# Optimization experiments

Hardware: AMD Instinct MI355X
Metric: run time of the kernel (lower is better)

## Reference

```python
import jax, jax.numpy as jnp
import numpy as np

HIDDEN = 64

def gcn_conv(x, W, b, src, dst, num_nodes):
    # GCNConv: out = D^{-1/2} (A + I) D^{-1/2} (x @ W) + b
    h = x @ W                                            # [N, F_out]
    ones = jnp.ones(src.shape[0], dtype=x.dtype)
    deg = jax.ops.segment_sum(ones, dst, num_segments=num_nodes) + 1.0  # +1 for self-loop
    dinv = jax.lax.rsqrt(deg)                             # deg^{-1/2}, deg >= 1 so safe
    norm = dinv[src] * dinv[dst]                          # [E]
    msgs = h[src] * norm[:, None]                         # [E, F_out]
    agg = jax.ops.segment_sum(msgs, dst, num_segments=num_nodes)
    # self-loop contribution: norm for (i,i) edge = dinv[i]^2
    out = agg + h * (dinv * dinv)[:, None] + b
    return out


def setup_inputs() -> dict:
    key = jax.random.key(0)
    k1, k2, k3, k4, k5 = jax.random.split(key, 5)
    N, F_in, F_out, E = 50000, 256, 128, 1600000
    x = jax.random.normal(k1, (N, F_in), dtype=jnp.float32)
    edge_index = jax.random.randint(k2, (2, E), 0, N, dtype=jnp.int64)
    W1 = jax.random.normal(k3, (F_in, HIDDEN), dtype=jnp.float32) * (1.0 / np.sqrt(F_in))
    b1 = jnp.zeros((HIDDEN,), dtype=jnp.float32)
    W2 = jax.random.normal(k4, (HIDDEN, F_out), dtype=jnp.float32) * (1.0 / np.sqrt(HIDDEN))
    b2 = jnp.zeros((F_out,), dtype=jnp.float32)
    return {"x": x, "edge_index": edge_index, "W1": W1, "b1": b1, "W2": W2, "b2": b2}


def reference(x, edge_index, W1, b1, W2, b2):
    num_nodes = x.shape[0]
    src, dst = edge_index[0], edge_index[1]
    h = gcn_conv(x, W1, b1, src, dst, num_nodes)
    h = jax.nn.relu(h)
    # dropout is identity in eval mode (training=False)
    out = gcn_conv(h, W2, b2, src, dst, num_nodes)
    return out
```

## Files before the change

kernel.cpp:

```cpp
#include <hip/hip_runtime.h>

#define FI 256
#define FH 64
#define FO 128
#define ASORT_CHUNK 2048

typedef __attribute__((ext_vector_type(8))) short bf16x8;
typedef __attribute__((ext_vector_type(4))) float f32x4;

__device__ __forceinline__ ushort f2bf(float x) {
    unsigned b = __float_as_uint(x);
    b += 0x7fffu + ((b >> 16) & 1u);
    return (ushort)(b >> 16);
}
__device__ __forceinline__ float bf2f(ushort u) {
    return __uint_as_float(((unsigned)u) << 16);
}


__global__ void zero_i32(int* __restrict__ p, int n) {
    int i = blockIdx.x * 256 + threadIdx.x;
    if (i < n) p[i] = 0;
}

__global__ void deg_cnt_kernel(const int* __restrict__ dst, int* __restrict__ cnt, int E) {
    int base = blockIdx.x * 1024 + threadIdx.x;
    #pragma unroll
    for (int q = 0; q < 4; ++q) {
        int e = base + q * 256;
        if (e < E) atomicAdd(&cnt[dst[e]], 1);
    }
}

__global__ void dinv_kernel(const int* __restrict__ cnt, float* __restrict__ dinv, int N) {
    int i = blockIdx.x * 256 + threadIdx.x;
    if (i < N) dinv[i] = rsqrtf((float)cnt[i] + 1.0f);
}


__global__ __launch_bounds__(256) void hist_wprep_kernel(const int* __restrict__ dst,
                                                         int* __restrict__ bucket_cnt,
                                                         const float* __restrict__ W1,
                                                         short* __restrict__ WH,
                                                         short* __restrict__ WL,
                                                         int E, int nblkA) {
    if ((int)blockIdx.x >= nblkA) {
        int f = ((int)blockIdx.x - nblkA) * 256 + threadIdx.x;
        float4 wv = *(const float4*)&W1[(size_t)f * 4];
        int k  = f >> 4;
        int c4 = f & 15;
        int j  = k & 7;
        int e0 = ((c4 >> 2) * 8 + (k >> 5)) * 64 + ((k >> 3) & 3) * 16 + (c4 & 3) * 4;
        float vv[4] = {wv.x, wv.y, wv.z, wv.w};
        #pragma unroll
        for (int cc = 0; cc < 4; ++cc) {
            ushort h = f2bf(vv[cc]);
            WH[(e0 + cc) * 8 + j] = (short)h;
            WL[(e0 + cc) * 8 + j] = (short)f2bf(vv[cc] - bf2f(h));
        }
        return;
    }
    __shared__ int lcnt[256];
    int t = threadIdx.x;
    int base = blockIdx.x * ASORT_CHUNK;
    lcnt[t] = 0;
    __syncthreads();
    #pragma unroll
    for (int j = 0; j < 8; ++j) {
        int e = base + j * 256 + t;
        if (e < E) atomicAdd(&lcnt[((unsigned)dst[e]) >> 8], 1);
    }
    __syncthreads();
    int v = lcnt[t];
    if (v > 0) atomicAdd(&bucket_cnt[t], v);
}

__global__ __launch_bounds__(256) void bucket_scan_kernel(const int* __restrict__ bucket_cnt,
                                                          int* __restrict__ bucket_base,
                                                          int* __restrict__ bucket_pos, int E) {
    __shared__ int sc[256];
    int t = threadIdx.x;
    int sum = bucket_cnt[t];
    sc[t] = sum;
    __syncthreads();
    for (int off = 1; off < 256; off <<= 1) {
        int u = (t >= off) ? sc[t - off] : 0;
        __syncthreads();
        sc[t] += u;
        __syncthreads();
    }
    int excl = sc[t] - sum;
    bucket_base[t] = excl;
    bucket_pos[t]  = excl;
    if (t == 255) bucket_base[256] = sc[255];
}

__global__ __launch_bounds__(256) void binA_kernel(const int* __restrict__ src,
                                                   const int* __restrict__ dst,
                                                   int* __restrict__ bucket_pos,
                                                   unsigned* __restrict__ binned, int E) {
    __shared__ int lcnt[256];
    __shared__ int lbase[256];
    __shared__ int gbase[256];
    __shared__ int sc[256];
    __shared__ unsigned sorted[ASORT_CHUNK];
    int t = threadIdx.x;
    int base = blockIdx.x * ASORT_CHUNK;
    lcnt[t] = 0;
    __syncthreads();
    unsigned pk[8];
    short bb[8];
    short mi[8];
    #pragma unroll
    for (int j = 0; j < 8; ++j) {
        int e = base + j * 256 + t;
        if (e < E) {
            unsigned s = (unsigned)src[e];
            unsigned d = (unsigned)dst[e];
            pk[j] = s | (d << 16);
            int b = (int)(d >> 8);
            bb[j] = (short)b;
            mi[j] = (short)atomicAdd(&lcnt[b], 1);
        } else {
            bb[j] = -1;
        }
    }
    __syncthreads();
    int v = lcnt[t];
    sc[t] = v;
    __syncthreads();
    #pragma unroll
    for (int off = 1; off < 256; off <<= 1) {
        int u = (t >= off) ? sc[t - off] : 0;
        __syncthreads();
        sc[t] += u;
        __syncthreads();
    }
    lbase[t] = sc[t] - v;
    if (v > 0) gbase[t] = atomicAdd(&bucket_pos[t], v);
    __syncthreads();
    #pragma unroll
    for (int j = 0; j < 8; ++j)
        if (bb[j] >= 0) sorted[lbase[(int)bb[j]] + (int)mi[j]] = pk[j];
    int tot = sc[255];
    __syncthreads();
    for (int i = t; i < tot; i += 256) {
        unsigned vv = sorted[i];
        int b = (int)(vv >> 24);
        binned[gbase[b] + (i - lbase[b])] = vv;
    }
}

__global__ __launch_bounds__(256) void binB_kernel(const int* __restrict__ bucket_base,
                                                   const unsigned* __restrict__ binned,
                                                   int* __restrict__ rec4,
                                                   int* __restrict__ row_start,
                                                   int* __restrict__ cnt,
                                                   float* __restrict__ dinv, int N) {
    __shared__ int lcnt[256];
    __shared__ int sc[256];
    __shared__ int lstart[256];
    __shared__ int loff[256];
    int t = threadIdx.x;
    int d0 = blockIdx.x << 8;
    int start = bucket_base[blockIdx.x];
    int end   = bucket_base[blockIdx.x + 1];
    lcnt[t] = 0;
    __syncthreads();
    for (int i = start + t; i < end; i += 256)
        atomicAdd(&lcnt[(binned[i] >> 16) & 0xffu], 1);
    __syncthreads();
    int v = lcnt[t];
    sc[t] = v;
    __syncthreads();
    for (int off = 1; off < 256; off <<= 1) {
        int u = (t >= off) ? sc[t - off] : 0;
        __syncthreads();
        sc[t] += u;
        __syncthreads();
    }
    int st = start + sc[t] - v;
    lstart[t] = st;
    loff[t] = 0;
    if (d0 + t < N) {
        row_start[d0 + t] = st;
        cnt[d0 + t] = v;
        dinv[d0 + t] = rsqrtf((float)v + 1.0f);
    }
    __syncthreads();
    int i = start + t;
    for (; i + 768 < end; i += 1024) {
        unsigned v0 = binned[i];
        unsigned v1 = binned[i + 256];
        unsigned v2 = binned[i + 512];
        unsigned v3 = binned[i + 768];
        int dA = (int)((v0 >> 16) & 0xffu); int kA = atomicAdd(&loff[dA], 1);
        rec4[lstart[dA] + kA] = (int)(v0 & 0xffffu);
        int dB = (int)((v1 >> 16) & 0xffu); int kB = atomicAdd(&loff[dB], 1);
        rec4[lstart[dB] + kB] = (int)(v1 & 0xffffu);
        int dC = (int)((v2 >> 16) & 0xffu); int kC = atomicAdd(&loff[dC], 1);
        rec4[lstart[dC] + kC] = (int)(v2 & 0xffffu);
        int dD = (int)((v3 >> 16) & 0xffu); int kD = atomicAdd(&loff[dD], 1);
        rec4[lstart[dD] + kD] = (int)(v3 & 0xffffu);
    }
    for (; i < end; i += 256) {
        unsigned v4 = binned[i];
        int d = (int)((v4 >> 16) & 0xffu);
        int k = atomicAdd(&loff[d], 1);
        rec4[lstart[d] + k] = (int)(v4 & 0xffffu);
    }
}


#define ACC8(hv, wt)                                                   \
    acc[0] = fmaf(__uint_as_float((hv).x << 16),         wt, acc[0]);  \
    acc[1] = fmaf(__uint_as_float((hv).x & 0xffff0000u), wt, acc[1]);  \
    acc[2] = fmaf(__uint_as_float((hv).y << 16),         wt, acc[2]);  \
    acc[3] = fmaf(__uint_as_float((hv).y & 0xffff0000u), wt, acc[3]);  \
    acc[4] = fmaf(__uint_as_float((hv).z << 16),         wt, acc[4]);  \
    acc[5] = fmaf(__uint_as_float((hv).z & 0xffff0000u), wt, acc[5]);  \
    acc[6] = fmaf(__uint_as_float((hv).w << 16),         wt, acc[6]);  \
    acc[7] = fmaf(__uint_as_float((hv).w & 0xffff0000u), wt, acc[7]);

#define GATHER_CHUNK(OFFS)                                                     \
    for (int c0 = 0; c0 < n; c0 += 64) {                                       \
        int idx_l = c0 + L;                                                    \
        int sreg = node;                                                       \
        float wreg = 0.f;                                                      \
        if (idx_l < n) {                                                       \
            sreg = rec4[beg + idx_l];                                          \
            wreg = dinv[sreg] * dvd;                                           \
        }                                                                      \
        int m = n - c0; if (m > 64) m = 64;                                    \
        int umax = (m + 7) >> 3;                                               \
        uint4 hv[8];                                                           \
        _Pragma("unroll")                                                      \
        for (int u = 0; u < 8; ++u) {                                          \
            if (u < umax) {                                                    \
                int sidx = __shfl(sreg, u * 8 + g, 64);                        \
                hv[u] = *(const uint4*)(hb + (size_t)sidx * 256 + (OFFS) + q * 8); \
            }                                                                  \
        }                                                                      \
        _Pragma("unroll")                                                      \
        for (int u = 0; u < 8; ++u) {                                          \
            if (u < umax) {                                                    \
                float wt = __shfl(wreg, u * 8 + g, 64);                        \
                ACC8(hv[u], wt)                                                \
            }                                                                  \
        }                                                                      \
    }

__global__ void gather_relu_kernel(const int* __restrict__ rec4, const int* __restrict__ row_start,
                                   const int* __restrict__ cnt, const float* __restrict__ dinv,
                                   const float* __restrict__ b1, float* __restrict__ out, int N) {
    int node = blockIdx.x * 4 + (threadIdx.x >> 6);
    if (node >= N) return;
    int L = threadIdx.x & 63;
    int g = L >> 3;
    int q = L & 7;
    const ushort* hb = (const ushort*)out;
    int beg = row_start[node];
    int n   = cnt[node];
    float dvd = dinv[node];
    float acc[8] = {0.f, 0.f, 0.f, 0.f, 0.f, 0.f, 0.f, 0.f};
    GATHER_CHUNK(128)
    #pragma unroll
    for (int off = 8; off < 64; off <<= 1)
        #pragma unroll
        for (int j = 0; j < 8; ++j)
            acc[j] += __shfl_xor(acc[j], off, 64);
    if (L < 8) {
        float dv2 = dvd * dvd;
        uint4 ho = *(const uint4*)(hb + (size_t)node * 256 + 128 + q * 8);
        float4 bl = *(const float4*)&b1[q * 8];
        float4 bh = *(const float4*)&b1[q * 8 + 4];
        float r0 = fmaxf(acc[0] + dv2 * __uint_as_float(ho.x << 16)         + bl.x, 0.f);
        float r1 = fmaxf(acc[1] + dv2 * __uint_as_float(ho.x & 0xffff0000u) + bl.y, 0.f);
        float r2 = fmaxf(acc[2] + dv2 * __uint_as_float(ho.y << 16)         + bl.z, 0.f);
        float r3 = fmaxf(acc[3] + dv2 * __uint_as_float(ho.y & 0xffff0000u) + bl.w, 0.f);
        float r4 = fmaxf(acc[4] + dv2 * __uint_as_float(ho.z << 16)         + bh.x, 0.f);
        float r5 = fmaxf(acc[5] + dv2 * __uint_as_float(ho.z & 0xffff0000u) + bh.y, 0.f);
        float r6 = fmaxf(acc[6] + dv2 * __uint_as_float(ho.w << 16)         + bh.z, 0.f);
        float r7 = fmaxf(acc[7] + dv2 * __uint_as_float(ho.w & 0xffff0000u) + bh.w, 0.f);
        uint4 st;
        st.x = (unsigned)f2bf(r0) | ((unsigned)f2bf(r1) << 16);
        st.y = (unsigned)f2bf(r2) | ((unsigned)f2bf(r3) << 16);
        st.z = (unsigned)f2bf(r4) | ((unsigned)f2bf(r5) << 16);
        st.w = (unsigned)f2bf(r6) | ((unsigned)f2bf(r7) << 16);
        *(uint4*)((ushort*)out + (size_t)node * 256 + 192 + q * 8) = st;
    }
}

__global__ void gather_comb_kernel(const int* __restrict__ rec4, const int* __restrict__ row_start,
                                   const int* __restrict__ cnt, const float* __restrict__ dinv,
                                   float* __restrict__ out, int N) {
    int node = blockIdx.x * 4 + (threadIdx.x >> 6);
    if (node >= N) return;
    int L = threadIdx.x & 63;
    int g = L >> 3;
    int q = L & 7;
    const ushort* hb = (const ushort*)out;
    int beg = row_start[node];
    int n   = cnt[node];
    float dvd = dinv[node];
    float acc[8] = {0.f, 0.f, 0.f, 0.f, 0.f, 0.f, 0.f, 0.f};
    GATHER_CHUNK(192)
    #pragma unroll
    for (int off = 8; off < 64; off <<= 1)
        #pragma unroll
        for (int j = 0; j < 8; ++j)
            acc[j] += __shfl_xor(acc[j], off, 64);
    if (L < 8) {
        float dv2 = dvd * dvd;
        uint4 ho = *(const uint4*)(hb + (size_t)node * 256 + 192 + q * 8);
        float4 o0, o1;
        o0.x = acc[0] + dv2 * __uint_as_float(ho.x << 16);
        o0.y = acc[1] + dv2 * __uint_as_float(ho.x & 0xffff0000u);
        o0.z = acc[2] + dv2 * __uint_as_float(ho.y << 16);
        o0.w = acc[3] + dv2 * __uint_as_float(ho.y & 0xffff0000u);
        o1.x = acc[4] + dv2 * __uint_as_float(ho.z << 16);
        o1.y = acc[5] + dv2 * __uint_as_float(ho.z & 0xffff0000u);
        o1.z = acc[6] + dv2 * __uint_as_float(ho.w << 16);
        o1.w = acc[7] + dv2 * __uint_as_float(ho.w & 0xffff0000u);
        *(float4*)&out[(size_t)node * FO + q * 8]     = o0;
        *(float4*)&out[(size_t)node * FO + q * 8 + 4] = o1;
    }
}


__global__ __launch_bounds__(256, 3) void mm1_mfma_g(const float* __restrict__ x,
                                                     const short* __restrict__ WH,
                                                     const short* __restrict__ WL,
                                                     float* __restrict__ out, int N) {
    int tid = threadIdx.x;
    int wid = tid >> 6;
    int l   = tid & 63;
    int R0  = blockIdx.x * 64;
    int rowA = R0 + wid * 16 + (l & 15);
    int kg   = l >> 4;
    const float* xr = x + (size_t)rowA * FI;
    bool ok = rowA < N;
    const float4 z4 = make_float4(0.f, 0.f, 0.f, 0.f);

    float4 xv[16];
    #pragma unroll
    for (int t = 0; t < 8; ++t) {
        int kb = t * 32 + kg * 8;
        xv[2 * t]     = ok ? *(const float4*)&xr[kb]     : z4;
        xv[2 * t + 1] = ok ? *(const float4*)&xr[kb + 4] : z4;
    }

    f32x4 acc[4];
    #pragma unroll
    for (int c = 0; c < 4; ++c) acc[c] = (f32x4){0.f, 0.f, 0.f, 0.f};

    bf16x8 fh[2][4], fl[2][4];
    #pragma unroll
    for (int c = 0; c < 4; ++c) {
        int e = (c * 8 + 0) * 64 + l;
        fh[0][c] = *(const bf16x8*)&WH[(size_t)e * 8];
        fl[0][c] = *(const bf16x8*)&WL[(size_t)e * 8];
    }

    #pragma unroll
    for (int t = 0; t < 8; ++t) {
        const int cur = t & 1, nxt = cur ^ 1;
        if (t < 7) {
            #pragma unroll
            for (int c = 0; c < 4; ++c) {
                int e = (c * 8 + (t + 1)) * 64 + l;
                fh[nxt][c] = *(const bf16x8*)&WH[(size_t)e * 8];
                fl[nxt][c] = *(const bf16x8*)&WL[(size_t)e * 8];
            }
        }
        bf16x8 ah, al;
        {
            float4 a0 = xv[2 * t], a1 = xv[2 * t + 1];
            float va[8] = {a0.x, a0.y, a0.z, a0.w, a1.x, a1.y, a1.z, a1.w};
            #pragma unroll
            for (int j = 0; j < 8; ++j) {
                ushort h = f2bf(va[j]);
                ah[j] = (short)h;
                al[j] = (short)f2bf(va[j] - bf2f(h));
            }
        }
        #pragma unroll
        for (int c = 0; c < 4; ++c) {
            acc[c] = __builtin_amdgcn_mfma_f32_16x16x32_bf16(ah, fh[cur][c], acc[c], 0, 0, 0);
            acc[c] = __builtin_amdgcn_mfma_f32_16x16x32_bf16(ah, fl[cur][c], acc[c], 0, 0, 0);
            acc[c] = __builtin_amdgcn_mfma_f32_16x16x32_bf16(al, fh[cur][c], acc[c], 0, 0, 0);
        }
    }
    {
        int rbase = R0 + wid * 16 + (l >> 4) * 4;
        #pragma unroll
        for (int r = 0; r < 4; ++r) {
            int row = rbase + r;
            if (row < N) {
                ushort* ob = (ushort*)out + (size_t)row * 256 + 128;
                #pragma unroll
                for (int c = 0; c < 4; ++c)
                    ob[c * 16 + (l & 15)] = f2bf(acc[c][r]);
            }
        }
    }
}

__global__ __launch_bounds__(512) void mm1_mfma(const float* __restrict__ x,
                                                const float* __restrict__ W1,
                                                float* __restrict__ out, int N) {
    __shared__ short bfH[2048 * 8];
    __shared__ short bfL[2048 * 8];
    int tid = threadIdx.x;
    #pragma unroll
    for (int i = 0; i < 8; ++i) {
        int f = i * 512 + tid;
        float4 wv = *(const float4*)&W1[(size_t)f * 4];
        int k  = f >> 4;
        int c4 = f & 15;
        int j  = k & 7;
        int e0 = ((c4 >> 2) * 8 + (k >> 5)) * 64 + ((k >> 3) & 3) * 16 + (c4 & 3) * 4;
        float vv[4] = {wv.x, wv.y, wv.z, wv.w};
        #pragma unroll
        for (int cc = 0; cc < 4; ++cc) {
            ushort h = f2bf(vv[cc]);
            bfH[(e0 + cc) * 8 + j] = (short)h;
            bfL[(e0 + cc) * 8 + j] = (short)f2bf(vv[cc] - bf2f(h));
        }
    }
    __syncthreads();
    int wid = tid >> 6;
    int l   = tid & 63;
    int R0  = blockIdx.x * 128;
    int rowA = R0 + wid * 16 + (l & 15);
    int kg   = l >> 4;
    const float* xr = x + (size_t)rowA * FI;
    bool ok = rowA < N;
    const float4 z4 = make_float4(0.f, 0.f, 0.f, 0.f);
    f32x4 acc[4];
    #pragma unroll
    for (int c = 0; c < 4; ++c) acc[c] = (f32x4){0.f, 0.f, 0.f, 0.f};
    float4 xa = ok ? *(const float4*)&xr[kg * 8]     : z4;
    float4 xb = ok ? *(const float4*)&xr[kg * 8 + 4] : z4;
    #pragma unroll
    for (int t = 0; t < 8; ++t) {
        bf16x8 ah, al;
        {
            float va[8] = {xa.x, xa.y, xa.z, xa.w, xb.x, xb.y, xb.z, xb.w};
            #pragma unroll
            for (int j = 0; j < 8; ++j) {
                ushort h = f2bf(va[j]);
                ah[j] = (short)h;
                al[j] = (short)f2bf(va[j] - bf2f(h));
            }
        }
        if (t < 7) {
            int kb = (t + 1) * 32 + kg * 8;
            xa = ok ? *(const float4*)&xr[kb]     : z4;
            xb = ok ? *(const float4*)&xr[kb + 4] : z4;
        }
        #pragma unroll
        for (int c = 0; c < 4; ++c) {
            int e = (c * 8 + t) * 64 + l;
            bf16x8 bh = *(const bf16x8*)&bfH[e * 8];
            bf16x8 bl = *(const bf16x8*)&bfL[e * 8];
            acc[c] = __builtin_amdgcn_mfma_f32_16x16x32_bf16(ah, bh, acc[c], 0, 0, 0);
            acc[c] = __builtin_amdgcn_mfma_f32_16x16x32_bf16(ah, bl, acc[c], 0, 0, 0);
            acc[c] = __builtin_amdgcn_mfma_f32_16x16x32_bf16(al, bh, acc[c], 0, 0, 0);
        }
    }
    {
        int rbase = R0 + wid * 16 + (l >> 4) * 4;
        #pragma unroll
        for (int r = 0; r < 4; ++r) {
            int row = rbase + r;
            if (row < N) {
                ushort* ob = (ushort*)out + (size_t)row * 256 + 128;
                #pragma unroll
                for (int c = 0; c < 4; ++c)
                    ob[c * 16 + (l & 15)] = f2bf(acc[c][r]);
            }
        }
    }
}

__global__ __launch_bounds__(256) void mm2_tiled(const float* __restrict__ W2,
                                                 const float* __restrict__ b2,
                                                 float* __restrict__ out, int N) {
    __shared__ float xs[64][68];
    __shared__ float ws[64][128];
    int tid = threadIdx.x;
    int R0  = blockIdx.x * 64;
    int ty  = tid >> 4;
    int tx  = tid & 15;

    {
        int sr = tid >> 2;
        int l4 = tid & 3;
        int grow = R0 + sr;
        bool ok = grow < N;
        const float* orow = out + (size_t)grow * FO;
        #pragma unroll
        for (int q = 0; q < 4; ++q) {
            int j0 = (l4 + 4 * q) * 4;
            float4 a = ok ? *(const float4*)&orow[j0] : make_float4(0.f, 0.f, 0.f, 0.f);
            xs[j0 + 0][sr] = a.x;
            xs[j0 + 1][sr] = a.y;
            xs[j0 + 2][sr] = a.z;
            xs[j0 + 3][sr] = a.w;
        }
    }
    #pragma unroll
    for (int q = 0; q < 8; ++q) {
        int f = tid + q * 256;
        *(float4*)&ws[f >> 5][(f & 31) * 4] = *(const float4*)&W2[(size_t)f * 4];
    }
    __syncthreads();

    float acc[4][8];
    #pragma unroll
    for (int i = 0; i < 4; ++i)
        #pragma unroll
        for (int j = 0; j < 8; ++j) acc[i][j] = 0.f;

    #pragma unroll 4
    for (int k = 0; k < FH; ++k) {
        float4 a  = *(const float4*)&xs[k][ty * 4];
        float4 bl = *(const float4*)&ws[k][tx * 4];
        float4 bh = *(const float4*)&ws[k][64 + tx * 4];
        float av[4] = {a.x, a.y, a.z, a.w};
        float bv[8] = {bl.x, bl.y, bl.z, bl.w, bh.x, bh.y, bh.z, bh.w};
        #pragma unroll
        for (int i = 0; i < 4; ++i)
            #pragma unroll
            for (int j = 0; j < 8; ++j)
                acc[i][j] = fmaf(av[i], bv[j], acc[i][j]);
    }

    float4 b2l = *(const float4*)&b2[tx * 4];
    float4 b2h = *(const float4*)&b2[64 + tx * 4];
    #pragma unroll
    for (int i = 0; i < 4; ++i) {
        int row = R0 + ty * 4 + i;
        if (row < N) {
            float* o = out + (size_t)row * FO;
            *(float4*)&o[tx * 4] = make_float4(acc[i][0] + b2l.x, acc[i][1] + b2l.y,
                                               acc[i][2] + b2l.z, acc[i][3] + b2l.w);
            *(float4*)&o[64 + tx * 4] = make_float4(acc[i][4] + b2h.x, acc[i][5] + b2h.y,
                                                    acc[i][6] + b2h.z, acc[i][7] + b2h.w);
        }
    }
}


__global__ void expand_hs1_kernel(float* __restrict__ out, int N) {
    int row = blockIdx.x * 4 + (threadIdx.x >> 6);
    if (row >= N) return;
    int lane = threadIdx.x & 63;
    float v = bf2f(((const ushort*)out)[(size_t)row * 256 + 128 + lane]);
    out[(size_t)row * FO + FH + lane] = v;
}

__global__ void zero_half_kernel(float* __restrict__ out, int half, int N) {
    int i = blockIdx.x * 256 + threadIdx.x;
    if (i >= N * FH) return;
    out[(size_t)(i >> 6) * FO + half + (i & 63)] = 0.f;
}

__global__ void scatter_half_kernel(const int* __restrict__ src, const int* __restrict__ dst,
                                    const float* __restrict__ dinv, float* __restrict__ out,
                                    int rh, int wh, int E) {
    int e = blockIdx.x * 4 + (threadIdx.x >> 6);
    if (e >= E) return;
    int lane = threadIdx.x & 63;
    int s = src[e];
    int d = dst[e];
    float w = dinv[s] * dinv[d];
    atomicAdd(&out[(size_t)d * FO + wh + lane], out[(size_t)s * FO + rh + lane] * w);
}

__global__ void finish1_kernel(float* __restrict__ out, const float* __restrict__ dinv,
                               const float* __restrict__ b1, int N) {
    int i = blockIdx.x * 256 + threadIdx.x;
    if (i >= N * FH) return;
    int row = i >> 6;
    int c   = i & 63;
    size_t base = (size_t)row * FO;
    float dv = dinv[row];
    out[base + c] = fmaxf(out[base + c] + dv * dv * out[base + FH + c] + b1[c], 0.f);
}

__global__ void finish2_kernel(float* __restrict__ out, const float* __restrict__ dinv, int N) {
    int i = blockIdx.x * 256 + threadIdx.x;
    if (i >= N * FH) return;
    int row = i >> 6;
    int c   = i & 63;
    size_t base = (size_t)row * FO;
    float dv = dinv[row];
    out[base + c] = out[base + FH + c] + dv * dv * out[base + c];
}

extern "C" void kernel_launch(void* const* d_in, const int* in_sizes, int n_in,
                              void* d_out, int out_size, void* d_ws, size_t ws_size,
                              hipStream_t stream) {
    const float* x  = (const float*)d_in[0];
    const int*   ei = (const int*)d_in[1];
    const float* W1 = (const float*)d_in[2];
    const float* b1 = (const float*)d_in[3];
    const float* W2 = (const float*)d_in[4];
    const float* b2 = (const float*)d_in[5];
    float* out = (float*)d_out;

    int N = in_sizes[0] / FI;
    int E = in_sizes[1] / 2;
    const int* src = ei;
    const int* dst = ei + E;

    char* w = (char*)d_ws;
    float* dinv        = (float*)w;      w += (size_t)N * 4;
    int*   cnt         = (int*)w;        w += (size_t)N * 4;
    int*   row_start   = (int*)w;        w += (size_t)N * 4;
    int*   bucket_cnt  = (int*)w;        w += 256 * 4;
    int*   bucket_pos  = (int*)w;        w += 256 * 4;
    int*   bucket_base = (int*)w;        w += 260 * 4;
    short* wfragH      = (short*)w;      w += 2048 * 8 * 2;
    short* wfragL      = (short*)w;      w += 2048 * 8 * 2;
    unsigned* binned   = (unsigned*)w;   w += (size_t)E * 4;
    int*   rec4        = (int*)w;        w += (size_t)E * 4;
    size_t need = (size_t)(w - (char*)d_ws);

    int nblkA = (E + ASORT_CHUNK - 1) / ASORT_CHUNK;
    int nbk   = (N + 255) >> 8;

    if (ws_size >= need && N <= 65536) {
        zero_i32<<<1, 256, 0, stream>>>(bucket_cnt, 256);
        hist_wprep_kernel<<<nblkA + 16, 256, 0, stream>>>(dst, bucket_cnt, W1, wfragH, wfragL, E, nblkA);
        bucket_scan_kernel<<<1, 256, 0, stream>>>(bucket_cnt, bucket_base, bucket_pos, E);
        binA_kernel<<<nblkA, 256, 0, stream>>>(src, dst, bucket_pos, binned, E);
        binB_kernel<<<nbk, 256, 0, stream>>>(bucket_base, binned, rec4, row_start, cnt, dinv, N);

        mm1_mfma_g<<<(N + 63) / 64, 256, 0, stream>>>(x, wfragH, wfragL, out, N);
        gather_relu_kernel<<<(N + 3) / 4, 256, 0, stream>>>(rec4, row_start, cnt, dinv, b1, out, N);
        gather_comb_kernel<<<(N + 3) / 4, 256, 0, stream>>>(rec4, row_start, cnt, dinv, out, N);
        mm2_tiled<<<(N + 63) / 64, 256, 0, stream>>>(W2, b2, out, N);
    } else {
        zero_i32<<<(N + 255) / 256, 256, 0, stream>>>(cnt, N);
        deg_cnt_kernel<<<(E + 1023) / 1024, 256, 0, stream>>>(dst, cnt, E);
        dinv_kernel<<<(N + 255) / 256, 256, 0, stream>>>(cnt, dinv, N);
        mm1_mfma<<<(N + 127) / 128, 512, 0, stream>>>(x, W1, out, N);
        expand_hs1_kernel<<<(N + 3) / 4, 256, 0, stream>>>(out, N);
        zero_half_kernel<<<((N * FH) + 255) / 256, 256, 0, stream>>>(out, 0, N);
        scatter_half_kernel<<<(E + 3) / 4, 256, 0, stream>>>(src, dst, dinv, out, FH, 0, E);
        finish1_kernel<<<((N * FH) + 255) / 256, 256, 0, stream>>>(out, dinv, b1, N);
        zero_half_kernel<<<((N * FH) + 255) / 256, 256, 0, stream>>>(out, FH, N);
        scatter_half_kernel<<<(E + 3) / 4, 256, 0, stream>>>(src, dst, dinv, out, 0, FH, E);
        finish2_kernel<<<((N * FH) + 255) / 256, 256, 0, stream>>>(out, dinv, N);
        mm2_tiled<<<(N + 63) / 64, 256, 0, stream>>>(W2, b2, out, N);
    }
}
```

Baseline: 280.3 us.

## Split mm1 output columns across waves instead of rows per wave

Each block now handles 16 rows, and each of its four waves computes one 16-column slice of the 64 hidden outputs. Before, each wave computed all 64 columns for its own 16 rows. This cuts per-wave accumulators and weight-fragment registers, allowing higher occupancy (launch bound raised to 4) and four times more blocks. In exchange, every wave in a block reloads the same 16 rows of x from global memory, so x traffic through the cache is multiplied by four.

```diff
diff --git a/kernel.cpp b/kernel.cpp
--- a/kernel.cpp
+++ b/kernel.cpp
@@ -328,15 +328,15 @@
 }
 
 
-__global__ __launch_bounds__(256, 3) void mm1_mfma_g(const float* __restrict__ x,
+__global__ __launch_bounds__(256, 4) void mm1_mfma_g(const float* __restrict__ x,
                                                      const short* __restrict__ WH,
                                                      const short* __restrict__ WL,
                                                      float* __restrict__ out, int N) {
     int tid = threadIdx.x;
     int wid = tid >> 6;
     int l   = tid & 63;
-    int R0  = blockIdx.x * 64;
-    int rowA = R0 + wid * 16 + (l & 15);
+    int R0  = blockIdx.x * 16;
+    int rowA = R0 + (l & 15);
     int kg   = l >> 4;
     const float* xr = x + (size_t)rowA * FI;
     bool ok = rowA < N;
@@ -350,28 +350,22 @@
         xv[2 * t + 1] = ok ? *(const float4*)&xr[kb + 4] : z4;
     }
 
-    f32x4 acc[4];
-    #pragma unroll
-    for (int c = 0; c < 4; ++c) acc[c] = (f32x4){0.f, 0.f, 0.f, 0.f};
-
-    bf16x8 fh[2][4], fl[2][4];
-    #pragma unroll
-    for (int c = 0; c < 4; ++c) {
-        int e = (c * 8 + 0) * 64 + l;
-        fh[0][c] = *(const bf16x8*)&WH[(size_t)e * 8];
-        fl[0][c] = *(const bf16x8*)&WL[(size_t)e * 8];
+    f32x4 acc = (f32x4){0.f, 0.f, 0.f, 0.f};
+
+    bf16x8 fh[2], fl[2];
+    {
+        int e = (wid * 8 + 0) * 64 + l;
+        fh[0] = *(const bf16x8*)&WH[(size_t)e * 8];
+        fl[0] = *(const bf16x8*)&WL[(size_t)e * 8];
     }
 
     #pragma unroll
     for (int t = 0; t < 8; ++t) {
         const int cur = t & 1, nxt = cur ^ 1;
         if (t < 7) {
-            #pragma unroll
-            for (int c = 0; c < 4; ++c) {
-                int e = (c * 8 + (t + 1)) * 64 + l;
-                fh[nxt][c] = *(const bf16x8*)&WH[(size_t)e * 8];
-                fl[nxt][c] = *(const bf16x8*)&WL[(size_t)e * 8];
-            }
+            int e = (wid * 8 + (t + 1)) * 64 + l;
+            fh[nxt] = *(const bf16x8*)&WH[(size_t)e * 8];
+            fl[nxt] = *(const bf16x8*)&WL[(size_t)e * 8];
         }
         bf16x8 ah, al;
         {
@@ -384,23 +378,18 @@
                 al[j] = (short)f2bf(va[j] - bf2f(h));
             }
         }
-        #pragma unroll
-        for (int c = 0; c < 4; ++c) {
-            acc[c] = __builtin_amdgcn_mfma_f32_16x16x32_bf16(ah, fh[cur][c], acc[c], 0, 0, 0);
-            acc[c] = __builtin_amdgcn_mfma_f32_16x16x32_bf16(ah, fl[cur][c], acc[c], 0, 0, 0);
-            acc[c] = __builtin_amdgcn_mfma_f32_16x16x32_bf16(al, fh[cur][c], acc[c], 0, 0, 0);
-        }
+        acc = __builtin_amdgcn_mfma_f32_16x16x32_bf16(ah, fh[cur], acc, 0, 0, 0);
+        acc = __builtin_amdgcn_mfma_f32_16x16x32_bf16(ah, fl[cur], acc, 0, 0, 0);
+        acc = __builtin_amdgcn_mfma_f32_16x16x32_bf16(al, fh[cur], acc, 0, 0, 0);
     }
     {
-        int rbase = R0 + wid * 16 + (l >> 4) * 4;
+        int rbase = R0 + (l >> 4) * 4;
         #pragma unroll
         for (int r = 0; r < 4; ++r) {
             int row = rbase + r;
             if (row < N) {
                 ushort* ob = (ushort*)out + (size_t)row * 256 + 128;
-                #pragma unroll
-                for (int c = 0; c < 4; ++c)
-                    ob[c * 16 + (l & 15)] = f2bf(acc[c][r]);
+                ob[wid * 16 + (l & 15)] = f2bf(acc[r]);
             }
         }
     }
@@ -639,7 +628,7 @@
         binA_kernel<<<nblkA, 256, 0, stream>>>(src, dst, bucket_pos, binned, E);
         binB_kernel<<<nbk, 256, 0, stream>>>(bucket_base, binned, rec4, row_start, cnt, dinv, N);
 
-        mm1_mfma_g<<<(N + 63) / 64, 256, 0, stream>>>(x, wfragH, wfragL, out, N);
+        mm1_mfma_g<<<(N + 15) / 16, 256, 0, stream>>>(x, wfragH, wfragL, out, N);
         gather_relu_kernel<<<(N + 3) / 4, 256, 0, stream>>>(rec4, row_start, cnt, dinv, b1, out, N);
         gather_comb_kernel<<<(N + 3) / 4, 256, 0, stream>>>(rec4, row_start, cnt, dinv, out, N);
         mm2_tiled<<<(N + 63) / 64, 256, 0, stream>>>(W2, b2, out, N);
```

Result: slower. 338.0 us (+20.6%).
